# Optimization experiments

Measured on AMD Instinct MI355X. Metric: run time of the kernel, lower is better.

Reference implementation:

```python
import jax, jax.numpy as jnp
import numpy as np

B, L, S, E, D = 16, 2048, 2048, 64, 64

def setup_inputs() -> dict:
    key = jax.random.key(0)
    k1, k2, k3, k4 = jax.random.split(key, 4)
    queries = jax.random.normal(k1, (B, L, E), dtype=jnp.float32)
    keys = jax.random.normal(k2, (B, S, E), dtype=jnp.float32)
    values = jax.random.normal(k3, (B, S, D), dtype=jnp.float32)
    mlp = jax.random.normal(k4, (L, L), dtype=jnp.float32)  # learned seq-mix matrix
    return {"queries": queries, "keys": keys, "values": values, "mlp": mlp}

def reference(queries, keys, values, mlp):
    # scale = 1/sqrt(E) (self.scale is None)
    E_dim = queries.shape[-1]
    scale = 1.0 / jnp.sqrt(jnp.asarray(E_dim, dtype=queries.dtype))
    # scores: [B, L, S]
    scores = jnp.einsum('ble,bse->bls', queries, keys)
    # dropout omitted (eval mode / attention_dropout=0)
    A = jax.nn.softmax(scale * scores, axis=-1)
    # attention output: [B, L, D]
    V = jnp.einsum('bls,bsd->bld', A, values)
    # learned sequence-mixing: [B, L, D] -> [B, P, D] with P == L
    out = jnp.einsum('bld,pl->bpd', V, mlp)
    return out
```

## Files before the change

kernel.cpp:

```cpp
#include <hip/hip_runtime.h>

#define NB 16
#define NL 2048
#define NS 2048
#define NE 64
#define ND 64

typedef float floatx4 __attribute__((ext_vector_type(4)));
typedef _Float16 half8 __attribute__((ext_vector_type(8)));
typedef __fp16 half2v __attribute__((ext_vector_type(2)));

union H8 { half8 v; half2v h2[4]; };

__device__ __forceinline__ half8 cvt8(floatx4 a, floatx4 b) {
  H8 h;
  h.h2[0] = __builtin_amdgcn_cvt_pkrtz(a[0], a[1]);
  h.h2[1] = __builtin_amdgcn_cvt_pkrtz(a[2], a[3]);
  h.h2[2] = __builtin_amdgcn_cvt_pkrtz(b[0], b[1]);
  h.h2[3] = __builtin_amdgcn_cvt_pkrtz(b[2], b[3]);
  return h.v;
}

__device__ __forceinline__ void async16(void* l, const void* g) {
  __builtin_amdgcn_global_load_lds((__attribute__((address_space(1))) void*)g,
                                   (__attribute__((address_space(3))) void*)l, 16, 0, 0);
}

__device__ __forceinline__ int kinv(int y) {
  return (y & 0x23) | ((y & 8) << 1) | ((y & 4) << 1) | ((y & 16) >> 2);
}

__global__ __launch_bounds__(256) void prep_k(const float* __restrict__ V,
                                              const float* __restrict__ K,
                                              _Float16* __restrict__ Vt,
                                              _Float16* __restrict__ Kh,
                                              int do_k) {
  __shared__ __align__(16) _Float16 Vl[64][72];
  const int bid = blockIdx.x;
  const int t = threadIdx.x;

  if (bid < 512) {
    const int b = bid >> 5;
    const int s0 = (bid & 31) * 64;
    {
      int sl = t & 63;
      int dg = t >> 6;
      const float* src = V + ((size_t)(b * NS + s0 + sl)) * ND + dg * 16;
      int x = kinv(sl);
      #pragma unroll
      for (int c = 0; c < 4; ++c) {
        floatx4 v = *(const floatx4*)(src + c * 4);
        #pragma unroll
        for (int e = 0; e < 4; ++e) Vl[dg * 16 + c * 4 + e][x] = (_Float16)v[e];
      }
    }
    __syncthreads();
    {
      int d = t & 63;
      int xg = t >> 6;
      int dk = (d & 7) << 3;
      #pragma unroll
      for (int h = 0; h < 2; ++h) {
        int x = xg * 16 + h * 8;
        half8 v = *(const half8*)&Vl[d][x];
        *(half8*)(Vt + ((size_t)(b * ND + d)) * NS + s0 + (x ^ dk)) = v;
      }
    }
  } else {
    if (!do_k) return;
    int c = (bid - 512) * 256 + t;
    int j = c & 7;
    int s = (c >> 3) & (NS - 1);
    int b = c >> 14;
    const float* src = K + ((size_t)(b * NS + s)) * NE + j * 8;
    half8 h = cvt8(*(const floatx4*)src, *(const floatx4*)(src + 4));
    *(half8*)(Kh + ((size_t)(b * NS + s)) * NE + (j ^ (s & 7)) * 8) = h;
  }
}

template<bool KH16>
__global__ __launch_bounds__(512) void attn_k(const float* __restrict__ Q,
                                              const void* __restrict__ Ksrc,
                                              const _Float16* __restrict__ Vtp,
                                              _Float16* __restrict__ Vatt,
                                              const float* __restrict__ Mf,
                                              _Float16* __restrict__ Mh) {
  __shared__ __align__(16) char smem[98304];
  const int tid = threadIdx.x;
  const int wid = tid >> 6, lane = tid & 63;
  const int lr = lane & 15, lg = lane >> 4;
  const int g = wid & 1;
  const int qh = wid >> 1;
  const int b = blockIdx.y;
  const int qbase = blockIdx.x * 128 + qh * 32;
  const _Float16* Kh = (const _Float16*)Ksrc;
  const float* Kf = (const float*)Ksrc;

  constexpr float SC = 0.18033688f;
  half8 qf[2][2];
  #pragma unroll
  for (int sub = 0; sub < 2; ++sub)
    #pragma unroll
    for (int kk = 0; kk < 2; ++kk) {
      const float* qp = Q + ((size_t)(b * NL + qbase + sub * 16 + lr)) * NE + kk * 32 + lg * 8;
      floatx4 a = *(const floatx4*)qp, c = *(const floatx4*)(qp + 4);
      qf[sub][kk] = cvt8(a * SC, c * SC);
    }

  half8 ones;
  #pragma unroll
  for (int i = 0; i < 8; ++i) ones[i] = (_Float16)1.0f;

  floatx4 oacc[2][4], lacc[2];
  #pragma unroll
  for (int s = 0; s < 2; ++s) {
    lacc[s] = (floatx4){0.f, 0.f, 0.f, 0.f};
    #pragma unroll
    for (int m = 0; m < 4; ++m) oacc[s][m] = (floatx4){0.f, 0.f, 0.f, 0.f};
  }

  int kOff[4][2], vOff[2][4];
  #pragma unroll
  for (int mt = 0; mt < 4; ++mt)
    #pragma unroll
    for (int kk = 0; kk < 2; ++kk) {
      int row = g * 64 + mt * 16 + lr, col = kk * 32 + lg * 8;
      kOff[mt][kk] = (row * 128 + col * 2) ^ ((row & 7) << 4);
    }
  #pragma unroll
  for (int kk = 0; kk < 2; ++kk)
    #pragma unroll
    for (int mt = 0; mt < 4; ++mt) {
      int row = mt * 16 + lr;
      vOff[kk][mt] = row * 256 + g * 128 + (((kk * 32 + lg * 8) * 2) ^ ((row & 7) << 4));
    }

  auto stageV = [&](int buf, int s0) {
    #pragma unroll
    for (int i = 0; i < 2; ++i) {
      int co = (wid * 2 + i) * 1024;
      int o = co + lane * 16;
      int row = o >> 8, c16 = (o >> 4) & 15;
      async16(smem + 49152 + buf * 16384 + co,
              Vtp + ((size_t)(b * ND + row)) * NS + s0 + c16 * 8);
    }
  };
  auto stageK = [&](int buf, int s0) {
    if constexpr (KH16) {
      #pragma unroll
      for (int i = 0; i < 2; ++i) {
        int co = (wid * 2 + i) * 1024;
        int o = co + lane * 16;
        int row = o >> 7, c8 = (o >> 4) & 7;
        async16(smem + buf * 16384 + co,
                Kh + ((size_t)(b * NS + s0 + row)) * NE + c8 * 8);
      }
    } else {
      int row = tid >> 2, cg = (tid & 3) * 16;
      const float* kp = Kf + ((size_t)(b * NS + s0 + row)) * NE + cg;
      #pragma unroll
      for (int c = 0; c < 2; ++c) {
        half8 h = cvt8(*(const floatx4*)(kp + c * 8), *(const floatx4*)(kp + c * 8 + 4));
        int col = cg + c * 8;
        *(half8*)(smem + buf * 16384 + ((row * 128 + col * 2) ^ ((row & 7) << 4))) = h;
      }
    }
  };

  stageK(0, 0); stageV(0, 0);

  int br = 0;
  for (int t = 0; t < NS / 128; ++t) {
    int bn = (br == 2) ? 0 : br + 1;
    if (t + 1 < NS / 128) {
      stageK(bn, (t + 1) * 128); stageV(bn, (t + 1) * 128);
      if constexpr (KH16) {
        asm volatile("s_waitcnt vmcnt(4)" ::: "memory");
        __builtin_amdgcn_s_barrier();
      } else __syncthreads();
    } else {
      if constexpr (KH16) {
        asm volatile("s_waitcnt vmcnt(0)" ::: "memory");
        __builtin_amdgcn_s_barrier();
      } else __syncthreads();
    }

    const char* kb = smem + br * 16384;
    const char* vb = smem + 49152 + br * 16384;

    half8 kf[4][2];
    #pragma unroll
    for (int mt = 0; mt < 4; ++mt)
      #pragma unroll
      for (int kk = 0; kk < 2; ++kk)
        kf[mt][kk] = *(const half8*)(kb + kOff[mt][kk]);

    H8 bf[2][2];
    #pragma unroll
    for (int sub = 0; sub < 2; ++sub) {
      floatx4 sacc[4];
      #pragma unroll
      for (int mt = 0; mt < 4; ++mt) sacc[mt] = (floatx4){0.f, 0.f, 0.f, 0.f};
      __builtin_amdgcn_s_setprio(1);
      #pragma unroll
      for (int kk = 0; kk < 2; ++kk)
        #pragma unroll
        for (int mt = 0; mt < 4; ++mt)
          sacc[mt] = __builtin_amdgcn_mfma_f32_16x16x32_f16(kf[mt][kk], qf[sub][kk], sacc[mt], 0, 0, 0);
      __builtin_amdgcn_s_setprio(0);

      #pragma unroll
      for (int mt = 0; mt < 4; ++mt) {
        float p0 = __builtin_amdgcn_exp2f(sacc[mt][0]);
        float p1 = __builtin_amdgcn_exp2f(sacc[mt][1]);
        float p2 = __builtin_amdgcn_exp2f(sacc[mt][2]);
        float p3 = __builtin_amdgcn_exp2f(sacc[mt][3]);
        bf[sub][mt >> 1].h2[(mt & 1) * 2]     = __builtin_amdgcn_cvt_pkrtz(p0, p1);
        bf[sub][mt >> 1].h2[(mt & 1) * 2 + 1] = __builtin_amdgcn_cvt_pkrtz(p2, p3);
      }
    }

    __builtin_amdgcn_s_setprio(1);
    #pragma unroll
    for (int kk = 0; kk < 2; ++kk) {
      #pragma unroll
      for (int mt = 0; mt < 4; ++mt) {
        half8 vt = *(const half8*)(vb + vOff[kk][mt]);
        oacc[0][mt] = __builtin_amdgcn_mfma_f32_16x16x32_f16(vt, bf[0][kk].v, oacc[0][mt], 0, 0, 0);
        oacc[1][mt] = __builtin_amdgcn_mfma_f32_16x16x32_f16(vt, bf[1][kk].v, oacc[1][mt], 0, 0, 0);
      }
      lacc[0] = __builtin_amdgcn_mfma_f32_16x16x32_f16(ones, bf[0][kk].v, lacc[0], 0, 0, 0);
      lacc[1] = __builtin_amdgcn_mfma_f32_16x16x32_f16(ones, bf[1][kk].v, lacc[1], 0, 0, 0);
    }
    __builtin_amdgcn_s_setprio(0);
    br = bn;
  }

  __syncthreads();

  {
    char* red = smem + qh * 12288;
    if (g == 1) {
      #pragma unroll
      for (int sub = 0; sub < 2; ++sub)
        #pragma unroll
        for (int mt = 0; mt < 4; ++mt)
          *(floatx4*)(red + lane * 144 + (sub * 4 + mt) * 16) = oacc[sub][mt];
      if (lg == 0) {
        *(float*)(red + 9216 + lr * 8) = lacc[0][0];
        *(float*)(red + 9216 + lr * 8 + 4) = lacc[1][0];
      }
    }
    __syncthreads();
    if (g == 0) {
      #pragma unroll
      for (int sub = 0; sub < 2; ++sub) {
        float lt = lacc[sub][0] + *(const float*)(red + 9216 + lr * 8 + sub * 4);
        float inv = __builtin_amdgcn_rcpf(lt);
        int l = qbase + sub * 16 + lr;
        #pragma unroll
        for (int mt = 0; mt < 4; ++mt) {
          floatx4 o = oacc[sub][mt] + *(const floatx4*)(red + lane * 144 + (sub * 4 + mt) * 16);
          #pragma unroll
          for (int r = 0; r < 4; ++r) {
            int d = mt * 16 + lg * 4 + r;
            int lsw = (l & ~63) | ((l & 63) ^ ((d & 7) << 3));
            Vatt[((size_t)(b * ND + d)) * NL + lsw] = (_Float16)(o[r] * inv);
          }
        }
      }
    }
  }

  if constexpr (KH16) {
    int mb = blockIdx.y * 16 + blockIdx.x;
    #pragma unroll
    for (int q = 0; q < 4; ++q) {
      int c = mb * 2048 + q * 512 + tid;
      int j = c & 255, p = c >> 8;
      const float* src = Mf + (size_t)p * NL + j * 8;
      half8 h = cvt8(*(const floatx4*)src, *(const floatx4*)(src + 4));
      int jo = (j & ~7) | ((j & 7) ^ (p & 7));
      *(half8*)(Mh + (size_t)p * NL + jo * 8) = h;
    }
  }
}

template<bool A16>
__global__ __launch_bounds__(256) void mix_k(const void* __restrict__ Asrc,
                                             const _Float16* __restrict__ Bsrc,
                                             float* __restrict__ out) {
  __shared__ __align__(16) char smem[98304];
  const int tid = threadIdx.x;
  const int wid = tid >> 6, lane = tid & 63;
  const int lr = lane & 15, lg = lane >> 4;
  const int kh = wid & 1;
  const int mw = wid >> 1;
  const int p0 = blockIdx.x * 64;
  const int b = blockIdx.y;
  const _Float16* Ah = (const _Float16*)Asrc;
  const float* Af = (const float*)Asrc;

  floatx4 acc[2][4];
  #pragma unroll
  for (int mt = 0; mt < 2; ++mt)
    #pragma unroll
    for (int nt = 0; nt < 4; ++nt) acc[mt][nt] = (floatx4){0.f, 0.f, 0.f, 0.f};

  auto stage = [&](int buf, int t) {
    int k0 = kh * (NL / 2) + t * 64;
    if constexpr (A16) {
      #pragma unroll
      for (int i = 0; i < 4; ++i) {
        int co = (mw * 4 + i) * 1024;
        int o = co + lane * 16;
        int row = o >> 7, c8 = (o >> 4) & 7;
        async16(smem + kh * 24576 + buf * 8192 + co,
                Ah + ((size_t)(p0 + row)) * NL + k0 + c8 * 8);
      }
    } else {
      int row = (lane & 31) + mw * 32, cg = (lane >> 5) * 32;
      const float* ap = Af + ((size_t)(p0 + row)) * NL + k0 + cg;
      #pragma unroll
      for (int c = 0; c < 4; ++c) {
        half8 h = cvt8(*(const floatx4*)(ap + c * 8), *(const floatx4*)(ap + c * 8 + 4));
        int col = cg + c * 8;
        *(half8*)(smem + kh * 24576 + buf * 8192 +
                  ((row * 128 + col * 2) ^ ((row & 7) << 4))) = h;
      }
    }
    #pragma unroll
    for (int i = 0; i < 4; ++i) {
      int co = (mw * 4 + i) * 1024;
      int o = co + lane * 16;
      int row = o >> 7, c8 = (o >> 4) & 7;
      async16(smem + 49152 + kh * 24576 + buf * 8192 + co,
              Bsrc + ((size_t)(b * ND + row)) * NL + k0 + c8 * 8);
    }
  };

  stage(0, 0);

  int br = 0;
  for (int t = 0; t < 16; ++t) {
    int bn = (br == 2) ? 0 : br + 1;
    if (t + 1 < 16) {
      stage(bn, t + 1);
      if constexpr (A16) {
        asm volatile("s_waitcnt vmcnt(8)" ::: "memory");
        __builtin_amdgcn_s_barrier();
      } else __syncthreads();
    } else {
      if constexpr (A16) {
        asm volatile("s_waitcnt vmcnt(0)" ::: "memory");
        __builtin_amdgcn_s_barrier();
      } else __syncthreads();
    }
    const char* ab = smem + kh * 24576 + br * 8192;
    const char* bb = smem + 49152 + kh * 24576 + br * 8192;
    #pragma unroll
    for (int kk = 0; kk < 2; ++kk) {
      int col = kk * 32 + lg * 8;
      half8 af[2];
      #pragma unroll
      for (int mt = 0; mt < 2; ++mt) {
        int row = mw * 32 + mt * 16 + lr;
        af[mt] = *(const half8*)(ab + ((row * 128 + col * 2) ^ ((row & 7) << 4)));
      }
      __builtin_amdgcn_s_setprio(1);
      #pragma unroll
      for (int nt = 0; nt < 4; ++nt) {
        int row = nt * 16 + lr;
        half8 bfr = *(const half8*)(bb + ((row * 128 + col * 2) ^ ((row & 7) << 4)));
        #pragma unroll
        for (int mt = 0; mt < 2; ++mt)
          acc[mt][nt] = __builtin_amdgcn_mfma_f32_16x16x32_f16(af[mt], bfr, acc[mt][nt], 0, 0, 0);
      }
      __builtin_amdgcn_s_setprio(0);
    }
    br = bn;
  }

  __syncthreads();

  if (kh == 1) {
    #pragma unroll
    for (int mt = 0; mt < 2; ++mt)
      #pragma unroll
      for (int nt = 0; nt < 4; ++nt) {
        int idx = mt * 4 + nt;
        *(floatx4*)(smem + mw * 8192 + lane * 128 + ((idx ^ (lane & 7)) * 16)) = acc[mt][nt];
      }
  }
  __syncthreads();
  if (kh == 0) {
    #pragma unroll
    for (int mt = 0; mt < 2; ++mt)
      #pragma unroll
      for (int nt = 0; nt < 4; ++nt) {
        int idx = mt * 4 + nt;
        acc[mt][nt] += *(const floatx4*)(smem + mw * 8192 + lane * 128 + ((idx ^ (lane & 7)) * 16));
        #pragma unroll
        for (int r = 0; r < 4; ++r) {
          int p = p0 + mw * 32 + mt * 16 + lg * 4 + r;
          int d = nt * 16 + lr;
          out[((size_t)(b * NL + p)) * ND + d] = acc[mt][nt][r];
        }
      }
  }
}

extern "C" void kernel_launch(void* const* d_in, const int* in_sizes, int n_in,
                              void* d_out, int out_size, void* d_ws, size_t ws_size,
                              hipStream_t stream) {
  (void)in_sizes; (void)n_in; (void)out_size;
  const float* Q = (const float*)d_in[0];
  const float* K = (const float*)d_in[1];
  const float* V = (const float*)d_in[2];
  const float* M = (const float*)d_in[3];
  float* out = (float*)d_out;

  char* ws = (char*)d_ws;
  _Float16* Vtp  = (_Float16*)ws;
  _Float16* Vatt = (_Float16*)(ws + (4u << 20));
  _Float16* Kh   = (_Float16*)(ws + (8u << 20));
  _Float16* Mh   = (_Float16*)(ws + (12u << 20));
  bool big = ws_size >= (size_t)(20u << 20);

  if (big) {
    prep_k<<<1536, 256, 0, stream>>>(V, K, Vtp, Kh, 1);
    attn_k<true><<<dim3(16, 16), 512, 0, stream>>>(Q, Kh, Vtp, Vatt, M, Mh);
    mix_k<true><<<dim3(32, 16), 256, 0, stream>>>(Mh, Vatt, out);
  } else {
    prep_k<<<512, 256, 0, stream>>>(V, K, Vtp, Kh, 0);
    attn_k<false><<<dim3(16, 16), 512, 0, stream>>>(Q, K, Vtp, Vatt, nullptr, nullptr);
    mix_k<false><<<dim3(32, 16), 256, 0, stream>>>(M, Vatt, out);
  }
}
```

Measured before the change: 55.25 us.

## Remap block indices for L2 locality and switch mix pipeline to double buffering

```diff
diff --git a/kernel.cpp b/kernel.cpp
--- a/kernel.cpp
+++ b/kernel.cpp
@@ -25,6 +25,10 @@
   __builtin_amdgcn_global_load_lds((__attribute__((address_space(1))) void*)g,
                                    (__attribute__((address_space(3))) void*)l, 16, 0, 0);
 }
+
+#define B1_WAIT8  { asm volatile("s_waitcnt vmcnt(8)" ::: "memory"); __builtin_amdgcn_s_barrier(); }
+#define B1_WAIT0  { asm volatile("s_waitcnt vmcnt(0)" ::: "memory"); __builtin_amdgcn_s_barrier(); }
+#define B2_LGKM   { asm volatile("s_waitcnt lgkmcnt(0)" ::: "memory"); __builtin_amdgcn_s_barrier(); }
 
 __device__ __forceinline__ int kinv(int y) {
   return (y & 0x23) | ((y & 8) << 1) | ((y & 4) << 1) | ((y & 16) >> 2);
@@ -91,8 +95,10 @@
   const int lr = lane & 15, lg = lane >> 4;
   const int g = wid & 1;
   const int qh = wid >> 1;
-  const int b = blockIdx.y;
-  const int qbase = blockIdx.x * 128 + qh * 32;
+  const int L = blockIdx.y * 16 + blockIdx.x;
+  const int b = (L & 7) * 2 + ((L >> 3) & 1);
+  const int qx = L >> 4;
+  const int qbase = qx * 128 + qh * 32;
   const _Float16* Kh = (const _Float16*)Ksrc;
   const float* Kf = (const float*)Ksrc;
 
@@ -290,14 +296,16 @@
 __global__ __launch_bounds__(256) void mix_k(const void* __restrict__ Asrc,
                                              const _Float16* __restrict__ Bsrc,
                                              float* __restrict__ out) {
-  __shared__ __align__(16) char smem[98304];
+  __shared__ __align__(16) char smem[65536];
   const int tid = threadIdx.x;
   const int wid = tid >> 6, lane = tid & 63;
   const int lr = lane & 15, lg = lane >> 4;
   const int kh = wid & 1;
   const int mw = wid >> 1;
-  const int p0 = blockIdx.x * 64;
-  const int b = blockIdx.y;
+  const int L = blockIdx.y * 32 + blockIdx.x;
+  const int i = L >> 3;
+  const int p0 = ((L & 7) * 4 + (i & 3)) * 64;
+  const int b = i >> 2;
   const _Float16* Ah = (const _Float16*)Asrc;
   const float* Af = (const float*)Asrc;
 
@@ -311,11 +319,11 @@
     int k0 = kh * (NL / 2) + t * 64;
     if constexpr (A16) {
       #pragma unroll
-      for (int i = 0; i < 4; ++i) {
-        int co = (mw * 4 + i) * 1024;
+      for (int i2 = 0; i2 < 4; ++i2) {
+        int co = (mw * 4 + i2) * 1024;
         int o = co + lane * 16;
         int row = o >> 7, c8 = (o >> 4) & 7;
-        async16(smem + kh * 24576 + buf * 8192 + co,
+        async16(smem + kh * 16384 + buf * 8192 + co,
                 Ah + ((size_t)(p0 + row)) * NL + k0 + c8 * 8);
       }
     } else {
@@ -325,39 +333,33 @@
       for (int c = 0; c < 4; ++c) {
         half8 h = cvt8(*(const floatx4*)(ap + c * 8), *(const floatx4*)(ap + c * 8 + 4));
         int col = cg + c * 8;
-        *(half8*)(smem + kh * 24576 + buf * 8192 +
+        *(half8*)(smem + kh * 16384 + buf * 8192 +
                   ((row * 128 + col * 2) ^ ((row & 7) << 4))) = h;
       }
     }
     #pragma unroll
-    for (int i = 0; i < 4; ++i) {
-      int co = (mw * 4 + i) * 1024;
+    for (int i2 = 0; i2 < 4; ++i2) {
+      int co = (mw * 4 + i2) * 1024;
       int o = co + lane * 16;
       int row = o >> 7, c8 = (o >> 4) & 7;
-      async16(smem + 49152 + kh * 24576 + buf * 8192 + co,
+      async16(smem + 32768 + kh * 16384 + buf * 8192 + co,
               Bsrc + ((size_t)(b * ND + row)) * NL + k0 + c8 * 8);
     }
   };
 
   stage(0, 0);
-
-  int br = 0;
+  if constexpr (!A16) __syncthreads();
+
   for (int t = 0; t < 16; ++t) {
-    int bn = (br == 2) ? 0 : br + 1;
+    int buf = t & 1;
     if (t + 1 < 16) {
-      stage(bn, t + 1);
-      if constexpr (A16) {
-        asm volatile("s_waitcnt vmcnt(8)" ::: "memory");
-        __builtin_amdgcn_s_barrier();
-      } else __syncthreads();
+      stage(buf ^ 1, t + 1);
+      if constexpr (A16) B1_WAIT8 else __syncthreads();
     } else {
-      if constexpr (A16) {
-        asm volatile("s_waitcnt vmcnt(0)" ::: "memory");
-        __builtin_amdgcn_s_barrier();
-      } else __syncthreads();
-    }
-    const char* ab = smem + kh * 24576 + br * 8192;
-    const char* bb = smem + 49152 + kh * 24576 + br * 8192;
+      if constexpr (A16) B1_WAIT0
+    }
+    const char* ab = smem + kh * 16384 + buf * 8192;
+    const char* bb = smem + 32768 + kh * 16384 + buf * 8192;
     #pragma unroll
     for (int kk = 0; kk < 2; ++kk) {
       int col = kk * 32 + lg * 8;
@@ -378,10 +380,8 @@
       }
       __builtin_amdgcn_s_setprio(0);
     }
-    br = bn;
-  }
-
-  __syncthreads();
+    if constexpr (A16) B2_LGKM else __syncthreads();
+  }
 
   if (kh == 1) {
     #pragma unroll
```

New measurement: 52.61 us. -4.8%, faster.
